# Kernel tuning notes

Hardware: AMD Instinct MI355X
Metric: run time of the kernel (lower is better)

The kernel has to match this reference:

```python
import jax, jax.numpy as jnp
import numpy as np

SEQ, DM, STATE, BATCH = 1024, 512, 16, 8
D2 = 2 * DM
EPS = 1e-5


def rmsnorm(x, w):
    return x * jax.lax.rsqrt(jnp.mean(x * x, axis=-1, keepdims=True) + EPS) * w


def setup_inputs() -> dict:
    key = jax.random.key(0)
    ks = jax.random.split(key, 16)
    def lin(k, i, o):
        k1, k2 = jax.random.split(k)
        s = 1.0 / np.sqrt(i)
        return (jax.random.uniform(k1, (i, o), minval=-s, maxval=s),
                jax.random.uniform(k2, (o,), minval=-s, maxval=s))
    inp_w, inp_b = lin(ks[0], DM, D2)
    convlin_w, convlin_b = lin(ks[1], D2, D2)
    fc1_w, fc1_b = lin(ks[2], D2, D2)
    fc2_w, fc2_b = lin(ks[3], D2, STATE)
    fc3_w, fc3_b = lin(ks[4], D2, STATE)
    D_w, D_b = lin(ks[5], DM, D2)
    out_w, _ = lin(ks[6], D2, DM)
    out_b = jnp.ones((DM,))  # nn.init.constant_(out_proj.bias, 1.0)
    # Conv1d(seq_len, seq_len, k=3): weight (out_ch=SEQ, in_ch=SEQ, 3)
    s = 1.0 / np.sqrt(SEQ * 3)
    conv_w = jax.random.uniform(ks[7], (SEQ, SEQ, 3), minval=-s, maxval=s)
    conv_b = jax.random.uniform(ks[8], (SEQ,), minval=-s, maxval=s)
    norm_w = jnp.ones((DM,))
    x = jax.random.normal(ks[9], (BATCH, SEQ, DM))
    return dict(x=x, norm_w=norm_w, inp_w=inp_w, inp_b=inp_b, conv_w=conv_w,
                conv_b=conv_b, convlin_w=convlin_w, convlin_b=convlin_b,
                fc1_w=fc1_w, fc1_b=fc1_b, fc2_w=fc2_w, fc2_b=fc2_b,
                fc3_w=fc3_w, fc3_b=fc3_b, D_w=D_w, D_b=D_b,
                out_w=out_w, out_b=out_b)


def reference(x, norm_w, inp_w, inp_b, conv_w, conv_b, convlin_w, convlin_b,
              fc1_w, fc1_b, fc2_w, fc2_b, fc3_w, fc3_b, D_w, D_b, out_w, out_b):
    xn = rmsnorm(x, norm_w)                                  # (b, L, d)
    x_proj = xn @ inp_w + inp_b                              # (b, L, 2d)
    # Conv1d over channels=seq_len, spatial=2d, padding=1
    x_conv = jax.lax.conv_general_dilated(
        x_proj, conv_w, window_strides=(1,), padding=[(1, 1)],
        dimension_numbers=('NCH', 'OIH', 'NCH')) + conv_b[None, :, None]
    x_conv_out = jax.nn.silu(x_conv) @ convlin_w + convlin_b  # (b, L, 2d)
    # S6: h starts at zero so dA term vanishes; y = x*delta*sum_n(B*C)
    u = x_conv_out
    B = u @ fc2_w + fc2_b                                     # (b, L, n)
    C = u @ fc3_w + fc3_b                                     # (b, L, n)
    delta = jax.nn.softplus(u @ fc1_w + fc1_b)                # (b, L, 2d)
    bc = jnp.sum(B * C, axis=-1, keepdims=True)               # (b, L, 1)
    x_ssm = u * delta * bc                                    # (b, L, 2d)
    x_act = jax.nn.silu(x_ssm)
    x_residual = jax.nn.silu(xn @ D_w + D_b)
    return (x_residual * x_act) @ out_w + out_b               # (b, L, d)
```

## Files before the change

kernel.cpp:

```cpp
#include <hip/hip_runtime.h>
#include <hip/hip_bf16.h>

#define SEQ 1024
#define DM 512
#define D2 1024
#define NSTATE 16
#define BATCH 8
#define ROWS (BATCH * SEQ)
#define EPSF 1e-5f

typedef __attribute__((ext_vector_type(8))) short bf16x8;
typedef __attribute__((ext_vector_type(4))) float f32x4;

#define AS1 __attribute__((address_space(1)))
#define AS3 __attribute__((address_space(3)))

__device__ __forceinline__ void gll16(const void* g, void* l) {
    __builtin_amdgcn_global_load_lds(
        (const AS1 unsigned int*)(uintptr_t)g,
        (AS3 unsigned int*)(unsigned int)(uintptr_t)l, 16, 0, 0);
}

__device__ __forceinline__ float sigmoidf_(float x) {
    return 1.f / (1.f + __expf(-x));
}
__device__ __forceinline__ unsigned short f2bf(float f) {
    __hip_bfloat16 h = __float2bfloat16(f);
    unsigned short r;
    __builtin_memcpy(&r, &h, 2);
    return r;
}

__global__ __launch_bounds__(256) void prep_all(
    const float* s0, const float* s1, const float* s2, const float* s3,
    const float* s4, const float* s5, const float* s6,
    __hip_bfloat16* d0, __hip_bfloat16* d1, __hip_bfloat16* d2,
    __hip_bfloat16* d3, __hip_bfloat16* d4, __hip_bfloat16* d5,
    __hip_bfloat16* d6) {
    const int j = blockIdx.z;
    int R, C;
    const float* src;
    __hip_bfloat16* dst;
    switch (j) {
        case 0: src = s0; dst = d0; R = 512; C = 1024; break;
        case 1: src = s1; dst = d1; R = 512; C = 1024; break;
        case 2: src = s2; dst = d2; R = 1024; C = 1024; break;
        case 3: src = s3; dst = d3; R = 1024; C = 1024; break;
        case 4: src = s4; dst = d4; R = 1024; C = 512; break;
        case 5: src = s5; dst = d5; R = 1024; C = 16; break;
        default: src = s6; dst = d6; R = 1024; C = 16; break;
    }
    int c0 = blockIdx.x * 32, r0 = blockIdx.y * 32;
    if (c0 >= C || r0 >= R) return;
    __shared__ float tile[32][33];
    int tx = threadIdx.x & 31, ty = threadIdx.x >> 5;
#pragma unroll
    for (int p = 0; p < 4; ++p) {
        int r = r0 + ty + p * 8, c = c0 + tx;
        if (r < R && c < C) tile[ty + p * 8][tx] = src[(size_t)r * C + c];
    }
    __syncthreads();
#pragma unroll
    for (int p = 0; p < 4; ++p) {
        int c = c0 + ty + p * 8, r = r0 + tx;
        if (r < R && c < C)
            dst[(size_t)c * R + r] = __float2bfloat16(tile[tx][ty + p * 8]);
    }
}

__global__ __launch_bounds__(256) void convw_k(const float* __restrict__ cw,
                                               __hip_bfloat16* __restrict__ wk) {
    int idx = blockIdx.x * 256 + threadIdx.x;
    float a = cw[(size_t)idx * 3 + 0];
    float b = cw[(size_t)idx * 3 + 1];
    float c = cw[(size_t)idx * 3 + 2];
    wk[idx] = __float2bfloat16(a);
    wk[(size_t)SEQ * SEQ + idx] = __float2bfloat16(b);
    wk[(size_t)2 * SEQ * SEQ + idx] = __float2bfloat16(c);
}

__global__ __launch_bounds__(256) void rmsnorm_k(
    const float* __restrict__ x, const float* __restrict__ w,
    __hip_bfloat16* __restrict__ o) {
    int row = blockIdx.x;
    const float* xr = x + (size_t)row * DM;
    __hip_bfloat16* orow = o + (size_t)row * DM;
    int t = threadIdx.x;
    float v0 = xr[t];
    float v1 = xr[t + 256];
    float ss = v0 * v0 + v1 * v1;
#pragma unroll
    for (int off = 32; off; off >>= 1) ss += __shfl_down(ss, off, 64);
    __shared__ float parts[4];
    if ((t & 63) == 0) parts[t >> 6] = ss;
    __syncthreads();
    float tot = parts[0] + parts[1] + parts[2] + parts[3];
    float rs = rsqrtf(tot * (1.f / DM) + EPSF);
    orow[t] = __float2bfloat16(v0 * rs * w[t]);
    orow[t + 256] = __float2bfloat16(v1 * rs * w[t + 256]);
}

template <int EPI, int KC>
__global__ __launch_bounds__(256) void mgemm(
    const __hip_bfloat16* __restrict__ A, const __hip_bfloat16* __restrict__ Bt,
    const float* __restrict__ bias, void* __restrict__ outp,
    void* __restrict__ outp2, const float* __restrict__ bias2,
    const __hip_bfloat16* __restrict__ uptr,
    const __hip_bfloat16* __restrict__ resid, const float* __restrict__ bcv,
    int M, int N) {
    __shared__ __align__(16) __hip_bfloat16 As[4][128 * 32];
    __shared__ __align__(16) __hip_bfloat16 Bs[4][128 * 32];
    const int nbx = gridDim.x;
    int lin = blockIdx.y * nbx + blockIdx.x;
    int chunk = (nbx * gridDim.y) >> 3;
    int wg = (lin & 7) * chunk + (lin >> 3);
    const int n0 = (wg % nbx) * 128, m0 = (wg / nbx) * 128;
    const int t = threadIdx.x, lane = t & 63, w = t >> 6;
    const int wr = w >> 1, wc = w & 1;
    const int l15 = lane & 15, l4 = lane >> 4;

    const int r0_ = t >> 2, c0_ = (t & 3) ^ ((r0_ >> 1) & 3);
    const int b1 = 256 + t, r1_ = b1 >> 2, c1_ = (b1 & 3) ^ ((r1_ >> 1) & 3);
    const __hip_bfloat16* gA0 = A + (size_t)(m0 + r0_) * KC + c0_ * 8;
    const __hip_bfloat16* gA1 = A + (size_t)(m0 + r1_) * KC + c1_ * 8;
    const __hip_bfloat16* gB0 = Bt + (size_t)(n0 + r0_) * KC + c0_ * 8;
    const __hip_bfloat16* gB1 = Bt + (size_t)(n0 + r1_) * KC + c1_ * 8;
    const int d0 = (w * 64) * 8, d1 = (256 + w * 64) * 8;

    int offA[4], offB[4];
#pragma unroll
    for (int i = 0; i < 4; ++i) {
        int ra = wr * 64 + i * 16 + l15;
        offA[i] = (ra * 4 + (l4 ^ ((ra >> 1) & 3))) * 8;
        int rb = wc * 64 + i * 16 + l15;
        offB[i] = (rb * 4 + (l4 ^ ((rb >> 1) & 3))) * 8;
    }

#define MSTAGE(BUF, K0)                  \
    {                                    \
        gll16(gA0 + (K0), &As[BUF][d0]); \
        gll16(gA1 + (K0), &As[BUF][d1]); \
        gll16(gB0 + (K0), &Bs[BUF][d0]); \
        gll16(gB1 + (K0), &Bs[BUF][d1]); \
    }

    f32x4 acc[4][4] = {};
    constexpr int NT = KC >> 6;
    MSTAGE(0, 0);
    MSTAGE(1, 32);
    asm volatile("s_waitcnt vmcnt(0)" ::: "memory");
    __builtin_amdgcn_s_barrier();
    __builtin_amdgcn_sched_barrier(0);

#pragma unroll 1
    for (int p = 0; p < NT; ++p) {
        const int kA = 2 * p, kB = 2 * p + 1;
        const int bufA = kA & 3, bufB = kB & 3;
        if (p + 1 < NT) {
            MSTAGE((kA + 2) & 3, (kA + 2) * 32);
            MSTAGE((kB + 2) & 3, (kB + 2) * 32);
        }
        bf16x8 a0[4], b0[4], a1[4], b1v[4];
#pragma unroll
        for (int i = 0; i < 4; ++i) {
            a0[i] = *(const bf16x8*)&As[bufA][offA[i]];
            b0[i] = *(const bf16x8*)&Bs[bufA][offB[i]];
        }
#pragma unroll
        for (int i = 0; i < 4; ++i) {
            a1[i] = *(const bf16x8*)&As[bufB][offA[i]];
            b1v[i] = *(const bf16x8*)&Bs[bufB][offB[i]];
        }
        __builtin_amdgcn_s_setprio(1);
#pragma unroll
        for (int i = 0; i < 4; ++i)
#pragma unroll
            for (int j = 0; j < 4; ++j)
                acc[i][j] = __builtin_amdgcn_mfma_f32_16x16x32_bf16(
                    a0[i], b0[j], acc[i][j], 0, 0, 0);
#pragma unroll
        for (int i = 0; i < 4; ++i)
#pragma unroll
            for (int j = 0; j < 4; ++j)
                acc[i][j] = __builtin_amdgcn_mfma_f32_16x16x32_bf16(
                    a1[i], b1v[j], acc[i][j], 0, 0, 0);
        __builtin_amdgcn_s_setprio(0);
        if (p + 1 < NT) {
            asm volatile("s_waitcnt vmcnt(0)" ::: "memory");
            __builtin_amdgcn_s_barrier();
            __builtin_amdgcn_sched_barrier(0);
        }
    }
#undef MSTAGE

    const int mb = m0 + wr * 64, nb = n0 + wc * 64;
#pragma unroll
    for (int i = 0; i < 4; ++i) {
#pragma unroll
        for (int j = 0; j < 4; ++j) {
            int ngl = nb + j * 16 + l15;
            if (EPI == 5) {
                if (nb < D2) {
                    float bj = bias[ngl];
                    int b = m0 >> 10;
                    int ibase = (mb & (SEQ - 1)) + i * 16 + l4 * 4;
                    ushort4 pk;
                    pk.x = f2bf(acc[i][j][0] + bj);
                    pk.y = f2bf(acc[i][j][1] + bj);
                    pk.z = f2bf(acc[i][j][2] + bj);
                    pk.w = f2bf(acc[i][j][3] + bj);
                    *(ushort4*)((__hip_bfloat16*)outp +
                                ((size_t)b * D2 + ngl) * SEQ + ibase) = pk;
                } else {
                    int ng2 = ngl - D2;
                    float bj = bias2[ng2];
#pragma unroll
                    for (int r = 0; r < 4; ++r) {
                        int mg = mb + i * 16 + l4 * 4 + r;
                        float c = acc[i][j][r] + bj;
                        ((__hip_bfloat16*)outp2)[(size_t)mg * D2 + ng2] =
                            __float2bfloat16(c * sigmoidf_(c));
                    }
                }
            } else {
                float bj = bias[ngl];
#pragma unroll
                for (int r = 0; r < 4; ++r) {
                    int mg = mb + i * 16 + l4 * 4 + r;
                    size_t ro = (size_t)mg * N + ngl;
                    float c = acc[i][j][r] + bj;
                    if (EPI == 1) {
                        ((__hip_bfloat16*)outp)[ro] = __float2bfloat16(c);
                    } else if (EPI == 3) {
                        float sp = (c > 20.f) ? c : log1pf(__expf(c));
                        float xs = __bfloat162float(uptr[ro]) * sp * bcv[mg];
                        float v = __bfloat162float(resid[ro]) *
                                  (xs * sigmoidf_(xs));
                        ((__hip_bfloat16*)outp)[ro] = __float2bfloat16(v);
                    } else {
                        ((float*)outp)[ro] = c;
                    }
                }
            }
        }
    }
}

__global__ __launch_bounds__(256) void conv_mfma(
    const __hip_bfloat16* __restrict__ wk,
    const __hip_bfloat16* __restrict__ Xt,
    const float* __restrict__ cb, __hip_bfloat16* __restrict__ outp) {
    __shared__ __align__(16) __hip_bfloat16 Ws[2][3][128 * 32];
    __shared__ __align__(16) __hip_bfloat16 Xs[2][128 * 32];
    __shared__ __align__(16) __hip_bfloat16 Xh[2][SEQ];
    int lin = blockIdx.x + 8 * blockIdx.y + 64 * blockIdx.z;
    int wg = (lin & 7) * 64 + (lin >> 3);
    const int n0 = (wg & 7) * 128;
    const int m0 = ((wg >> 3) & 7) * 128;
    const int z = wg >> 6;
    const int t = threadIdx.x, lane = t & 63, w = t >> 6;
    const int wr = w >> 1, wc = w & 1;
    const int l15 = lane & 15, l4 = lane >> 4;
    const __hip_bfloat16* Xtb = Xt + (size_t)z * D2 * SEQ;

    {
        int which = t >> 7;
        int col = (t & 127) * 8;
        int h = n0 - 1 + which * 129;
        uint4 v = make_uint4(0u, 0u, 0u, 0u);
        if (h >= 0 && h < D2)
            v = *(const uint4*)(Xtb + (size_t)h * SEQ + col);
        *(uint4*)&Xh[which][col] = v;
    }

    int rowp[2], cbw[2];
#pragma unroll
    for (int p = 0; p < 2; ++p) {
        int blk = p * 256 + t;
        rowp[p] = blk >> 2;
        cbw[p] = (blk & 3) ^ ((rowp[p] >> 1) & 3);
    }
    const __hip_bfloat16* wsrc[2][3];
    const __hip_bfloat16* xsrc[2];
#pragma unroll
    for (int p = 0; p < 2; ++p) {
#pragma unroll
        for (int tp = 0; tp < 3; ++tp)
            wsrc[p][tp] = wk + (size_t)tp * SEQ * SEQ +
                          (size_t)(m0 + rowp[p]) * SEQ + cbw[p] * 8;
        xsrc[p] = Xtb + (size_t)(n0 + rowp[p]) * SEQ + cbw[p] * 8;
    }
    const int dst0 = (w * 64) * 8, dst1 = (256 + w * 64) * 8;

    int offA[4];
#pragma unroll
    for (int i = 0; i < 4; ++i) {
        int ra = wr * 64 + i * 16 + l15;
        offA[i] = (ra * 4 + (l4 ^ ((ra >> 1) & 3))) * 8;
    }

#define CSTAGE(BUF, K0)                              \
    {                                                \
        gll16(wsrc[0][0] + (K0), &Ws[BUF][0][dst0]); \
        gll16(wsrc[1][0] + (K0), &Ws[BUF][0][dst1]); \
        gll16(wsrc[0][1] + (K0), &Ws[BUF][1][dst0]); \
        gll16(wsrc[1][1] + (K0), &Ws[BUF][1][dst1]); \
        gll16(wsrc[0][2] + (K0), &Ws[BUF][2][dst0]); \
        gll16(wsrc[1][2] + (K0), &Ws[BUF][2][dst1]); \
        gll16(xsrc[0] + (K0), &Xs[BUF][dst0]);       \
        gll16(xsrc[1] + (K0), &Xs[BUF][dst1]);       \
    }

    f32x4 acc[4][4] = {};
    CSTAGE(0, 0);
    asm volatile("s_waitcnt lgkmcnt(0)" ::: "memory");

#pragma unroll 1
    for (int kt = 0; kt < 32; ++kt) {
        const int k0 = kt * 32;
        const int buf = kt & 1;
        if (kt + 1 < 32) {
            CSTAGE(buf ^ 1, (kt + 1) * 32);
            asm volatile("s_waitcnt vmcnt(8)" ::: "memory");
        } else {
            asm volatile("s_waitcnt vmcnt(0)" ::: "memory");
        }
        __builtin_amdgcn_s_barrier();
        __builtin_amdgcn_sched_barrier(0);
        bf16x8 aw[3][4];
#pragma unroll
        for (int tp = 0; tp < 3; ++tp)
#pragma unroll
            for (int i = 0; i < 4; ++i)
                aw[tp][i] = *(const bf16x8*)&Ws[buf][tp][offA[i]];
        __builtin_amdgcn_s_setprio(1);
#pragma unroll
        for (int j = 0; j < 4; ++j) {
#pragma unroll
            for (int tp = 0; tp < 3; ++tp) {
                int rb = wc * 64 + j * 16 + l15 + tp;
                int r = rb - 1;
                const __hip_bfloat16* src =
                    &Xs[buf][(r * 4 + (l4 ^ ((r >> 1) & 3))) * 8];
                if (rb == 0) src = &Xh[0][k0 + l4 * 8];
                if (rb == 129) src = &Xh[1][k0 + l4 * 8];
                bf16x8 bvx = *(const bf16x8*)src;
#pragma unroll
                for (int i = 0; i < 4; ++i)
                    acc[i][j] = __builtin_amdgcn_mfma_f32_16x16x32_bf16(
                        aw[tp][i], bvx, acc[i][j], 0, 0, 0);
            }
        }
        __builtin_amdgcn_s_setprio(0);
        if (kt + 1 < 32) {
            __builtin_amdgcn_s_barrier();
            __builtin_amdgcn_sched_barrier(0);
        }
    }
#undef CSTAGE

    const int mb = m0 + wr * 64, nb = n0 + wc * 64;
    size_t ob = (size_t)z * SEQ * D2;
#pragma unroll
    for (int i = 0; i < 4; ++i)
#pragma unroll
        for (int j = 0; j < 4; ++j)
#pragma unroll
            for (int r = 0; r < 4; ++r) {
                int mg = mb + i * 16 + l4 * 4 + r;
                int ng = nb + j * 16 + l15;
                float c = acc[i][j][r] + cb[mg];
                outp[ob + (size_t)mg * D2 + ng] =
                    __float2bfloat16(c * sigmoidf_(c));
            }
}

__global__ __launch_bounds__(256) void bc2_k(
    const __hip_bfloat16* __restrict__ u, const __hip_bfloat16* __restrict__ fcT,
    const float* __restrict__ b2, const float* __restrict__ b3,
    float* __restrict__ bc) {
    __shared__ __align__(16) __hip_bfloat16 Bl[32 * 1024];
    __shared__ __align__(16) __hip_bfloat16 As[3][128 * 32];
    const int m0 = blockIdx.x * 128;
    const int t = threadIdx.x, lane = t & 63, w = t >> 6;
    const int l15 = lane & 15, l4 = lane >> 4;

#pragma unroll
    for (int it = 0; it < 16; ++it) {
        int q = it * 256 + t;
        int n = q >> 7, blk = q & 127;
        uint4 v = *(const uint4*)(fcT + (size_t)n * 1024 + blk * 8);
        *(uint4*)&Bl[(n * 128 + (blk ^ (n & 7))) * 8] = v;
    }

    const int r0_ = t >> 2, c0_ = (t & 3) ^ ((r0_ >> 1) & 3);
    const int bq = 256 + t, r1_ = bq >> 2, c1_ = (bq & 3) ^ ((r1_ >> 1) & 3);
    const __hip_bfloat16* gA0 = u + (size_t)(m0 + r0_) * 1024 + c0_ * 8;
    const __hip_bfloat16* gA1 = u + (size_t)(m0 + r1_) * 1024 + c1_ * 8;
    const int d0 = (w * 64) * 8, d1 = (256 + w * 64) * 8;

    int offA[2];
#pragma unroll
    for (int i = 0; i < 2; ++i) {
        int ra = w * 32 + i * 16 + l15;
        offA[i] = (ra * 4 + (l4 ^ ((ra >> 1) & 3))) * 8;
    }

#define BSTAGE(BUF, K0)                  \
    {                                    \
        gll16(gA0 + (K0), &As[BUF][d0]); \
        gll16(gA1 + (K0), &As[BUF][d1]); \
    }

    f32x4 acc[2][2] = {};
    unsigned curb = 0, nxtb = 1, thdb = 2;
    BSTAGE(0, 0);
    BSTAGE(1, 32);
    asm volatile("s_waitcnt vmcnt(2)" ::: "memory");
    __builtin_amdgcn_s_barrier();
    __builtin_amdgcn_sched_barrier(0);

#pragma unroll 1
    for (int kt = 0; kt < 32; ++kt) {
        const bool st = (kt + 2 < 32);
        if (st) BSTAGE(thdb, (kt + 2) * 32);
        bf16x8 af[2], bf[2];
#pragma unroll
        for (int i = 0; i < 2; ++i) af[i] = *(const bf16x8*)&As[curb][offA[i]];
#pragma unroll
        for (int nj = 0; nj < 2; ++nj) {
            int n = nj * 16 + l15;
            int blk = (kt * 4 + l4) ^ (n & 7);
            bf[nj] = *(const bf16x8*)&Bl[(n * 128 + blk) * 8];
        }
#pragma unroll
        for (int i = 0; i < 2; ++i)
#pragma unroll
            for (int nj = 0; nj < 2; ++nj)
                acc[i][nj] = __builtin_amdgcn_mfma_f32_16x16x32_bf16(
                    af[i], bf[nj], acc[i][nj], 0, 0, 0);
        if (kt + 1 < 32) {
            if (st)
                asm volatile("s_waitcnt vmcnt(2)" ::: "memory");
            else
                asm volatile("s_waitcnt vmcnt(0)" ::: "memory");
            __builtin_amdgcn_s_barrier();
            __builtin_amdgcn_sched_barrier(0);
        }
        unsigned tb = curb;
        curb = nxtb;
        nxtb = thdb;
        thdb = tb;
    }
#undef BSTAGE

    float bb2 = b2[l15], bb3 = b3[l15];
#pragma unroll
    for (int i = 0; i < 2; ++i)
#pragma unroll
        for (int r = 0; r < 4; ++r) {
            float Bv = acc[i][0][r] + bb2;
            float Cv = acc[i][1][r] + bb3;
            float p = Bv * Cv;
            p += __shfl_xor(p, 1, 64);
            p += __shfl_xor(p, 2, 64);
            p += __shfl_xor(p, 4, 64);
            p += __shfl_xor(p, 8, 64);
            if (l15 == 0)
                bc[m0 + w * 32 + i * 16 + l4 * 4 + r] = p;
        }
}

extern "C" void kernel_launch(void* const* d_in, const int* in_sizes, int n_in,
                              void* d_out, int out_size, void* d_ws,
                              size_t ws_size, hipStream_t stream) {
    const float* x = (const float*)d_in[0];
    const float* norm_w = (const float*)d_in[1];
    const float* inp_w = (const float*)d_in[2];
    const float* inp_b = (const float*)d_in[3];
    const float* conv_w = (const float*)d_in[4];
    const float* conv_b = (const float*)d_in[5];
    const float* convlin_w = (const float*)d_in[6];
    const float* convlin_b = (const float*)d_in[7];
    const float* fc1_w = (const float*)d_in[8];
    const float* fc1_b = (const float*)d_in[9];
    const float* fc2_w = (const float*)d_in[10];
    const float* fc2_b = (const float*)d_in[11];
    const float* fc3_w = (const float*)d_in[12];
    const float* fc3_b = (const float*)d_in[13];
    const float* D_w = (const float*)d_in[14];
    const float* D_b = (const float*)d_in[15];
    const float* out_w = (const float*)d_in[16];
    const float* out_b = (const float*)d_in[17];
    float* out = (float*)d_out;

    __hip_bfloat16* xnb = (__hip_bfloat16*)d_ws;
    __hip_bfloat16* xt = xnb + (size_t)ROWS * DM;
    __hip_bfloat16* cvo = xt + (size_t)BATCH * D2 * SEQ;
    __hip_bfloat16* u = cvo + (size_t)ROWS * D2;
    __hip_bfloat16* resid = u + (size_t)ROWS * D2;
    __hip_bfloat16* Wcat = resid + (size_t)ROWS * D2;
    __hip_bfloat16* clT = Wcat + (size_t)2 * D2 * DM;
    __hip_bfloat16* fc1T = clT + (size_t)D2 * D2;
    __hip_bfloat16* outT = fc1T + (size_t)D2 * D2;
    __hip_bfloat16* wk = outT + (size_t)DM * D2;
    __hip_bfloat16* fcT = wk + (size_t)3 * SEQ * SEQ;
    float* bcb = (float*)(fcT + (size_t)32 * D2);

    prep_all<<<dim3(32, 32, 7), 256, 0, stream>>>(
        inp_w, D_w, convlin_w, fc1_w, out_w, fc2_w, fc3_w, Wcat,
        Wcat + (size_t)D2 * DM, clT, fc1T, outT, fcT, fcT + (size_t)16 * D2);
    convw_k<<<SEQ * SEQ / 256, 256, 0, stream>>>(conv_w, wk);
    rmsnorm_k<<<ROWS, 256, 0, stream>>>(x, norm_w, xnb);
    mgemm<5, DM><<<dim3(2 * D2 / 128, ROWS / 128), 256, 0, stream>>>(
        xnb, Wcat, inp_b, xt, resid, D_b, nullptr, nullptr, nullptr, ROWS,
        2 * D2);
    conv_mfma<<<dim3(D2 / 128, SEQ / 128, BATCH), 256, 0, stream>>>(
        wk, xt, conv_b, cvo);
    mgemm<1, D2><<<dim3(D2 / 128, ROWS / 128), 256, 0, stream>>>(
        cvo, clT, convlin_b, u, nullptr, nullptr, nullptr, nullptr, nullptr,
        ROWS, D2);
    bc2_k<<<ROWS / 128, 256, 0, stream>>>(u, fcT, fc2_b, fc3_b, bcb);
    mgemm<3, D2><<<dim3(D2 / 128, ROWS / 128), 256, 0, stream>>>(
        u, fc1T, fc1_b, cvo, nullptr, nullptr, u, resid, bcb, ROWS, D2);
    mgemm<4, D2><<<dim3(DM / 128, ROWS / 128), 256, 0, stream>>>(
        cvo, outT, out_b, out, nullptr, nullptr, nullptr, nullptr, nullptr,
        ROWS, DM);
}
```

Baseline: 224.4 us.

## Fold convlin weights into fc1/fc2/fc3 and fuse u and delta GEMMs

```diff
diff --git a/kernel.cpp b/kernel.cpp
--- a/kernel.cpp
+++ b/kernel.cpp
@@ -24,20 +24,54 @@
 __device__ __forceinline__ float sigmoidf_(float x) {
     return 1.f / (1.f + __expf(-x));
 }
+__device__ __forceinline__ float softplusf_(float x) {
+    return fmaxf(x, 0.f) + __logf(1.f + __expf(-fabsf(x)));
+}
 __device__ __forceinline__ unsigned short f2bf(float f) {
     __hip_bfloat16 h = __float2bfloat16(f);
     unsigned short r;
     __builtin_memcpy(&r, &h, 2);
     return r;
 }
+__device__ __forceinline__ float bf2f(__hip_bfloat16 h) {
+    return __bfloat162float(h);
+}
+__device__ __forceinline__ float bfbits2f(short s) {
+    return __uint_as_float(((unsigned)(unsigned short)s) << 16);
+}
 
 __global__ __launch_bounds__(256) void prep_all(
     const float* s0, const float* s1, const float* s2, const float* s3,
-    const float* s4, const float* s5, const float* s6,
-    __hip_bfloat16* d0, __hip_bfloat16* d1, __hip_bfloat16* d2,
-    __hip_bfloat16* d3, __hip_bfloat16* d4, __hip_bfloat16* d5,
-    __hip_bfloat16* d6) {
+    const float* s4, const float* s5, const float* s6, const float* clw,
+    const float* cw, __hip_bfloat16* d0, __hip_bfloat16* d1,
+    __hip_bfloat16* d2, __hip_bfloat16* d3, __hip_bfloat16* d4,
+    __hip_bfloat16* d5, __hip_bfloat16* d6, __hip_bfloat16* clB,
+    __hip_bfloat16* wk) {
     const int j = blockIdx.z;
+    if (j == 8) {
+        int bid = blockIdx.y * 32 + blockIdx.x;
+        int base = bid * 1024 + threadIdx.x;
+#pragma unroll
+        for (int it = 0; it < 4; ++it) {
+            int idx = base + it * 256;
+            wk[idx] = __float2bfloat16(cw[(size_t)idx * 3 + 0]);
+            wk[(size_t)SEQ * SEQ + idx] =
+                __float2bfloat16(cw[(size_t)idx * 3 + 1]);
+            wk[(size_t)2 * SEQ * SEQ + idx] =
+                __float2bfloat16(cw[(size_t)idx * 3 + 2]);
+        }
+        return;
+    }
+    if (j == 7) {
+        int c0 = blockIdx.x * 32, r0 = blockIdx.y * 32;
+        int tx = threadIdx.x & 31, ty = threadIdx.x >> 5;
+#pragma unroll
+        for (int p = 0; p < 4; ++p) {
+            int r = r0 + ty + p * 8, c = c0 + tx;
+            clB[(size_t)r * D2 + c] = __float2bfloat16(clw[(size_t)r * D2 + c]);
+        }
+        return;
+    }
     int R, C;
     const float* src;
     __hip_bfloat16* dst;
@@ -68,15 +102,46 @@
     }
 }
 
-__global__ __launch_bounds__(256) void convw_k(const float* __restrict__ cw,
-                                               __hip_bfloat16* __restrict__ wk) {
-    int idx = blockIdx.x * 256 + threadIdx.x;
-    float a = cw[(size_t)idx * 3 + 0];
-    float b = cw[(size_t)idx * 3 + 1];
-    float c = cw[(size_t)idx * 3 + 2];
-    wk[idx] = __float2bfloat16(a);
-    wk[(size_t)SEQ * SEQ + idx] = __float2bfloat16(b);
-    wk[(size_t)2 * SEQ * SEQ + idx] = __float2bfloat16(c);
+__global__ __launch_bounds__(256) void biasprep_k(
+    const float* __restrict__ clb, const float* __restrict__ fc1w,
+    const float* __restrict__ fc1b, const float* __restrict__ fc2w,
+    const float* __restrict__ fc2b, const float* __restrict__ fc3w,
+    const float* __restrict__ fc3b, float* __restrict__ b1p,
+    float* __restrict__ b23p) {
+    int g = blockIdx.x * 256 + threadIdx.x;
+    if (g < 1024) {
+        float acc = 0.f;
+        for (int k = 0; k < 1024; ++k) acc += clb[k] * fc1w[(size_t)k * 1024 + g];
+        b1p[g] = acc + fc1b[g];
+    } else if (g < 1040) {
+        int s = g - 1024;
+        float acc = 0.f;
+        for (int k = 0; k < 1024; ++k) acc += clb[k] * fc2w[k * 16 + s];
+        b23p[s] = acc + fc2b[s];
+    } else if (g < 1056) {
+        int s = g - 1040;
+        float acc = 0.f;
+        for (int k = 0; k < 1024; ++k) acc += clb[k] * fc3w[k * 16 + s];
+        b23p[16 + s] = acc + fc3b[s];
+    }
+}
+
+__global__ __launch_bounds__(256) void prepw23_k(
+    const __hip_bfloat16* __restrict__ clB, const __hip_bfloat16* __restrict__ fcT,
+    __hip_bfloat16* __restrict__ W2pT) {
+    int g = blockIdx.x * 256 + threadIdx.x;
+    int k = g >> 5, s = g & 31;
+    const __hip_bfloat16* ck = clB + (size_t)k * 1024;
+    const __hip_bfloat16* fs = fcT + (size_t)s * 1024;
+    float acc = 0.f;
+    for (int j = 0; j < 1024; j += 8) {
+        bf16x8 a = *(const bf16x8*)&ck[j];
+        bf16x8 b = *(const bf16x8*)&fs[j];
+#pragma unroll
+        for (int e = 0; e < 8; ++e)
+            acc += bfbits2f(a[e]) * bfbits2f(b[e]);
+    }
+    W2pT[(size_t)s * 1024 + k] = __float2bfloat16(acc);
 }
 
 __global__ __launch_bounds__(256) void rmsnorm_k(
@@ -104,10 +169,7 @@
 __global__ __launch_bounds__(256) void mgemm(
     const __hip_bfloat16* __restrict__ A, const __hip_bfloat16* __restrict__ Bt,
     const float* __restrict__ bias, void* __restrict__ outp,
-    void* __restrict__ outp2, const float* __restrict__ bias2,
-    const __hip_bfloat16* __restrict__ uptr,
-    const __hip_bfloat16* __restrict__ resid, const float* __restrict__ bcv,
-    int M, int N) {
+    void* __restrict__ outp2, const float* __restrict__ bias2, int M, int N) {
     __shared__ __align__(16) __hip_bfloat16 As[4][128 * 32];
     __shared__ __align__(16) __hip_bfloat16 Bs[4][128 * 32];
     const int nbx = gridDim.x;
@@ -223,20 +285,14 @@
                     }
                 }
             } else {
-                float bj = bias[ngl];
+                float bj = (EPI == 6) ? 0.f : bias[ngl];
 #pragma unroll
                 for (int r = 0; r < 4; ++r) {
                     int mg = mb + i * 16 + l4 * 4 + r;
                     size_t ro = (size_t)mg * N + ngl;
                     float c = acc[i][j][r] + bj;
-                    if (EPI == 1) {
+                    if (EPI == 6) {
                         ((__hip_bfloat16*)outp)[ro] = __float2bfloat16(c);
-                    } else if (EPI == 3) {
-                        float sp = (c > 20.f) ? c : log1pf(__expf(c));
-                        float xs = __bfloat162float(uptr[ro]) * sp * bcv[mg];
-                        float v = __bfloat162float(resid[ro]) *
-                                  (xs * sigmoidf_(xs));
-                        ((__hip_bfloat16*)outp)[ro] = __float2bfloat16(v);
                     } else {
                         ((float*)outp)[ro] = c;
                     }
@@ -244,6 +300,214 @@
             }
         }
     }
+}
+
+__global__ __launch_bounds__(256) void fused_ud(
+    const __hip_bfloat16* __restrict__ A, const __hip_bfloat16* __restrict__ BtU,
+    const __hip_bfloat16* __restrict__ BtD, const float* __restrict__ biasU,
+    const float* __restrict__ biasD, const __hip_bfloat16* __restrict__ resid,
+    const float* __restrict__ bcv, __hip_bfloat16* __restrict__ act) {
+    __shared__ __align__(16) __hip_bfloat16 As[2][128 * 32];
+    __shared__ __align__(16) __hip_bfloat16 Bu[2][128 * 32];
+    __shared__ __align__(16) __hip_bfloat16 Bd[2][128 * 32];
+    const int nbx = gridDim.x;
+    int lin = blockIdx.y * nbx + blockIdx.x;
+    int chunk = (nbx * gridDim.y) >> 3;
+    int wg = (lin & 7) * chunk + (lin >> 3);
+    const int n0 = (wg % nbx) * 128, m0 = (wg / nbx) * 128;
+    const int t = threadIdx.x, lane = t & 63, w = t >> 6;
+    const int wr = w >> 1, wc = w & 1;
+    const int l15 = lane & 15, l4 = lane >> 4;
+
+    const int r0_ = t >> 2, c0_ = (t & 3) ^ ((r0_ >> 1) & 3);
+    const int b1 = 256 + t, r1_ = b1 >> 2, c1_ = (b1 & 3) ^ ((r1_ >> 1) & 3);
+    const __hip_bfloat16* gA0 = A + (size_t)(m0 + r0_) * D2 + c0_ * 8;
+    const __hip_bfloat16* gA1 = A + (size_t)(m0 + r1_) * D2 + c1_ * 8;
+    const __hip_bfloat16* gU0 = BtU + (size_t)(n0 + r0_) * D2 + c0_ * 8;
+    const __hip_bfloat16* gU1 = BtU + (size_t)(n0 + r1_) * D2 + c1_ * 8;
+    const __hip_bfloat16* gD0 = BtD + (size_t)(n0 + r0_) * D2 + c0_ * 8;
+    const __hip_bfloat16* gD1 = BtD + (size_t)(n0 + r1_) * D2 + c1_ * 8;
+    const int d0 = (w * 64) * 8, d1 = (256 + w * 64) * 8;
+
+    int offA[4], offB[4];
+#pragma unroll
+    for (int i = 0; i < 4; ++i) {
+        int ra = wr * 64 + i * 16 + l15;
+        offA[i] = (ra * 4 + (l4 ^ ((ra >> 1) & 3))) * 8;
+        int rb = wc * 64 + i * 16 + l15;
+        offB[i] = (rb * 4 + (l4 ^ ((rb >> 1) & 3))) * 8;
+    }
+
+#define FSTAGE(BUF, K0)                  \
+    {                                    \
+        gll16(gA0 + (K0), &As[BUF][d0]); \
+        gll16(gA1 + (K0), &As[BUF][d1]); \
+        gll16(gU0 + (K0), &Bu[BUF][d0]); \
+        gll16(gU1 + (K0), &Bu[BUF][d1]); \
+        gll16(gD0 + (K0), &Bd[BUF][d0]); \
+        gll16(gD1 + (K0), &Bd[BUF][d1]); \
+    }
+
+    f32x4 accU[4][4] = {};
+    f32x4 accD[4][4] = {};
+    FSTAGE(0, 0);
+
+#pragma unroll 1
+    for (int kt = 0; kt < 32; ++kt) {
+        const int buf = kt & 1;
+        if (kt + 1 < 32) {
+            FSTAGE(buf ^ 1, (kt + 1) * 32);
+            asm volatile("s_waitcnt vmcnt(6)" ::: "memory");
+        } else {
+            asm volatile("s_waitcnt vmcnt(0)" ::: "memory");
+        }
+        __builtin_amdgcn_s_barrier();
+        __builtin_amdgcn_sched_barrier(0);
+        bf16x8 af[4], bu[4], bd[4];
+#pragma unroll
+        for (int i = 0; i < 4; ++i) {
+            af[i] = *(const bf16x8*)&As[buf][offA[i]];
+            bu[i] = *(const bf16x8*)&Bu[buf][offB[i]];
+            bd[i] = *(const bf16x8*)&Bd[buf][offB[i]];
+        }
+        __builtin_amdgcn_s_setprio(1);
+#pragma unroll
+        for (int i = 0; i < 4; ++i)
+#pragma unroll
+            for (int j = 0; j < 4; ++j)
+                accU[i][j] = __builtin_amdgcn_mfma_f32_16x16x32_bf16(
+                    af[i], bu[j], accU[i][j], 0, 0, 0);
+#pragma unroll
+        for (int i = 0; i < 4; ++i)
+#pragma unroll
+            for (int j = 0; j < 4; ++j)
+                accD[i][j] = __builtin_amdgcn_mfma_f32_16x16x32_bf16(
+                    af[i], bd[j], accD[i][j], 0, 0, 0);
+        __builtin_amdgcn_s_setprio(0);
+        if (kt + 1 < 32) {
+            __builtin_amdgcn_s_barrier();
+            __builtin_amdgcn_sched_barrier(0);
+        }
+    }
+#undef FSTAGE
+
+    const int mb = m0 + wr * 64, nb = n0 + wc * 64;
+#pragma unroll
+    for (int i = 0; i < 4; ++i) {
+#pragma unroll
+        for (int j = 0; j < 4; ++j) {
+            int ngl = nb + j * 16 + l15;
+            float bU = biasU[ngl];
+            float bD = biasD[ngl];
+#pragma unroll
+            for (int r = 0; r < 4; ++r) {
+                int mg = mb + i * 16 + l4 * 4 + r;
+                size_t ro = (size_t)mg * D2 + ngl;
+                float cu = accU[i][j][r] + bU;
+                float cd = accD[i][j][r] + bD;
+                float sp = softplusf_(cd);
+                float xs = cu * sp * bcv[mg];
+                float v = bf2f(resid[ro]) * (xs * sigmoidf_(xs));
+                act[ro] = __float2bfloat16(v);
+            }
+        }
+    }
+}
+
+__global__ __launch_bounds__(256) void bc2_k(
+    const __hip_bfloat16* __restrict__ u, const __hip_bfloat16* __restrict__ fcT,
+    const float* __restrict__ b2, const float* __restrict__ b3,
+    float* __restrict__ bc) {
+    __shared__ __align__(16) __hip_bfloat16 Bl[32 * 1024];
+    __shared__ __align__(16) __hip_bfloat16 As[3][128 * 32];
+    const int m0 = blockIdx.x * 128;
+    const int t = threadIdx.x, lane = t & 63, w = t >> 6;
+    const int l15 = lane & 15, l4 = lane >> 4;
+
+#pragma unroll
+    for (int it = 0; it < 16; ++it) {
+        int q = it * 256 + t;
+        int n = q >> 7, blk = q & 127;
+        uint4 v = *(const uint4*)(fcT + (size_t)n * 1024 + blk * 8);
+        *(uint4*)&Bl[(n * 128 + (blk ^ (n & 7))) * 8] = v;
+    }
+
+    const int r0_ = t >> 2, c0_ = (t & 3) ^ ((r0_ >> 1) & 3);
+    const int bq = 256 + t, r1_ = bq >> 2, c1_ = (bq & 3) ^ ((r1_ >> 1) & 3);
+    const __hip_bfloat16* gA0 = u + (size_t)(m0 + r0_) * 1024 + c0_ * 8;
+    const __hip_bfloat16* gA1 = u + (size_t)(m0 + r1_) * 1024 + c1_ * 8;
+    const int d0 = (w * 64) * 8, d1 = (256 + w * 64) * 8;
+
+    int offA[2];
+#pragma unroll
+    for (int i = 0; i < 2; ++i) {
+        int ra = w * 32 + i * 16 + l15;
+        offA[i] = (ra * 4 + (l4 ^ ((ra >> 1) & 3))) * 8;
+    }
+
+#define BSTAGE(BUF, K0)                  \
+    {                                    \
+        gll16(gA0 + (K0), &As[BUF][d0]); \
+        gll16(gA1 + (K0), &As[BUF][d1]); \
+    }
+
+    f32x4 acc[2][2] = {};
+    unsigned curb = 0, nxtb = 1, thdb = 2;
+    BSTAGE(0, 0);
+    BSTAGE(1, 32);
+    asm volatile("s_waitcnt vmcnt(2)" ::: "memory");
+    __builtin_amdgcn_s_barrier();
+    __builtin_amdgcn_sched_barrier(0);
+
+#pragma unroll 1
+    for (int kt = 0; kt < 32; ++kt) {
+        const bool st = (kt + 2 < 32);
+        if (st) BSTAGE(thdb, (kt + 2) * 32);
+        bf16x8 af[2], bf[2];
+#pragma unroll
+        for (int i = 0; i < 2; ++i) af[i] = *(const bf16x8*)&As[curb][offA[i]];
+#pragma unroll
+        for (int nj = 0; nj < 2; ++nj) {
+            int n = nj * 16 + l15;
+            int blk = (kt * 4 + l4) ^ (n & 7);
+            bf[nj] = *(const bf16x8*)&Bl[(n * 128 + blk) * 8];
+        }
+#pragma unroll
+        for (int i = 0; i < 2; ++i)
+#pragma unroll
+            for (int nj = 0; nj < 2; ++nj)
+                acc[i][nj] = __builtin_amdgcn_mfma_f32_16x16x32_bf16(
+                    af[i], bf[nj], acc[i][nj], 0, 0, 0);
+        if (kt + 1 < 32) {
+            if (st)
+                asm volatile("s_waitcnt vmcnt(2)" ::: "memory");
+            else
+                asm volatile("s_waitcnt vmcnt(0)" ::: "memory");
+            __builtin_amdgcn_s_barrier();
+            __builtin_amdgcn_sched_barrier(0);
+        }
+        unsigned tb = curb;
+        curb = nxtb;
+        nxtb = thdb;
+        thdb = tb;
+    }
+#undef BSTAGE
+
+    float bb2 = b2[l15], bb3 = b3[l15];
+#pragma unroll
+    for (int i = 0; i < 2; ++i)
+#pragma unroll
+        for (int r = 0; r < 4; ++r) {
+            float Bv = acc[i][0][r] + bb2;
+            float Cv = acc[i][1][r] + bb3;
+            float p = Bv * Cv;
+            p += __shfl_xor(p, 1, 64);
+            p += __shfl_xor(p, 2, 64);
+            p += __shfl_xor(p, 4, 64);
+            p += __shfl_xor(p, 8, 64);
+            if (l15 == 0)
+                bc[m0 + w * 32 + i * 16 + l4 * 4 + r] = p;
+        }
 }
 
 __global__ __launch_bounds__(256) void conv_mfma(
@@ -373,102 +637,6 @@
                 outp[ob + (size_t)mg * D2 + ng] =
                     __float2bfloat16(c * sigmoidf_(c));
             }
-}
-
-__global__ __launch_bounds__(256) void bc2_k(
-    const __hip_bfloat16* __restrict__ u, const __hip_bfloat16* __restrict__ fcT,
-    const float* __restrict__ b2, const float* __restrict__ b3,
-    float* __restrict__ bc) {
-    __shared__ __align__(16) __hip_bfloat16 Bl[32 * 1024];
-    __shared__ __align__(16) __hip_bfloat16 As[3][128 * 32];
-    const int m0 = blockIdx.x * 128;
-    const int t = threadIdx.x, lane = t & 63, w = t >> 6;
-    const int l15 = lane & 15, l4 = lane >> 4;
-
-#pragma unroll
-    for (int it = 0; it < 16; ++it) {
-        int q = it * 256 + t;
-        int n = q >> 7, blk = q & 127;
-        uint4 v = *(const uint4*)(fcT + (size_t)n * 1024 + blk * 8);
-        *(uint4*)&Bl[(n * 128 + (blk ^ (n & 7))) * 8] = v;
-    }
-
-    const int r0_ = t >> 2, c0_ = (t & 3) ^ ((r0_ >> 1) & 3);
-    const int bq = 256 + t, r1_ = bq >> 2, c1_ = (bq & 3) ^ ((r1_ >> 1) & 3);
-    const __hip_bfloat16* gA0 = u + (size_t)(m0 + r0_) * 1024 + c0_ * 8;
-    const __hip_bfloat16* gA1 = u + (size_t)(m0 + r1_) * 1024 + c1_ * 8;
-    const int d0 = (w * 64) * 8, d1 = (256 + w * 64) * 8;
-
-    int offA[2];
-#pragma unroll
-    for (int i = 0; i < 2; ++i) {
-        int ra = w * 32 + i * 16 + l15;
-        offA[i] = (ra * 4 + (l4 ^ ((ra >> 1) & 3))) * 8;
-    }
-
-#define BSTAGE(BUF, K0)                  \
-    {                                    \
-        gll16(gA0 + (K0), &As[BUF][d0]); \
-        gll16(gA1 + (K0), &As[BUF][d1]); \
-    }
-
-    f32x4 acc[2][2] = {};
-    unsigned curb = 0, nxtb = 1, thdb = 2;
-    BSTAGE(0, 0);
-    BSTAGE(1, 32);
-    asm volatile("s_waitcnt vmcnt(2)" ::: "memory");
-    __builtin_amdgcn_s_barrier();
-    __builtin_amdgcn_sched_barrier(0);
-
-#pragma unroll 1
-    for (int kt = 0; kt < 32; ++kt) {
-        const bool st = (kt + 2 < 32);
-        if (st) BSTAGE(thdb, (kt + 2) * 32);
-        bf16x8 af[2], bf[2];
-#pragma unroll
-        for (int i = 0; i < 2; ++i) af[i] = *(const bf16x8*)&As[curb][offA[i]];
-#pragma unroll
-        for (int nj = 0; nj < 2; ++nj) {
-            int n = nj * 16 + l15;
-            int blk = (kt * 4 + l4) ^ (n & 7);
-            bf[nj] = *(const bf16x8*)&Bl[(n * 128 + blk) * 8];
-        }
-#pragma unroll
-        for (int i = 0; i < 2; ++i)
-#pragma unroll
-            for (int nj = 0; nj < 2; ++nj)
-                acc[i][nj] = __builtin_amdgcn_mfma_f32_16x16x32_bf16(
-                    af[i], bf[nj], acc[i][nj], 0, 0, 0);
-        if (kt + 1 < 32) {
-            if (st)
-                asm volatile("s_waitcnt vmcnt(2)" ::: "memory");
-            else
-                asm volatile("s_waitcnt vmcnt(0)" ::: "memory");
-            __builtin_amdgcn_s_barrier();
-            __builtin_amdgcn_sched_barrier(0);
-        }
-        unsigned tb = curb;
-        curb = nxtb;
-        nxtb = thdb;
-        thdb = tb;
-    }
-#undef BSTAGE
-
-    float bb2 = b2[l15], bb3 = b3[l15];
-#pragma unroll
-    for (int i = 0; i < 2; ++i)
-#pragma unroll
-        for (int r = 0; r < 4; ++r) {
-            float Bv = acc[i][0][r] + bb2;
-            float Cv = acc[i][1][r] + bb3;
-            float p = Bv * Cv;
-            p += __shfl_xor(p, 1, 64);
-            p += __shfl_xor(p, 2, 64);
-            p += __shfl_xor(p, 4, 64);
-            p += __shfl_xor(p, 8, 64);
-            if (l15 == 0)
-                bc[m0 + w * 32 + i * 16 + l4 * 4 + r] = p;
-        }
 }
 
 extern "C" void kernel_launch(void* const* d_in, const int* in_sizes, int n_in,
@@ -497,33 +665,38 @@
     __hip_bfloat16* xnb = (__hip_bfloat16*)d_ws;
     __hip_bfloat16* xt = xnb + (size_t)ROWS * DM;
     __hip_bfloat16* cvo = xt + (size_t)BATCH * D2 * SEQ;
-    __hip_bfloat16* u = cvo + (size_t)ROWS * D2;
-    __hip_bfloat16* resid = u + (size_t)ROWS * D2;
+    __hip_bfloat16* act = cvo + (size_t)ROWS * D2;
+    __hip_bfloat16* resid = act + (size_t)ROWS * D2;
     __hip_bfloat16* Wcat = resid + (size_t)ROWS * D2;
     __hip_bfloat16* clT = Wcat + (size_t)2 * D2 * DM;
     __hip_bfloat16* fc1T = clT + (size_t)D2 * D2;
     __hip_bfloat16* outT = fc1T + (size_t)D2 * D2;
     __hip_bfloat16* wk = outT + (size_t)DM * D2;
     __hip_bfloat16* fcT = wk + (size_t)3 * SEQ * SEQ;
-    float* bcb = (float*)(fcT + (size_t)32 * D2);
-
-    prep_all<<<dim3(32, 32, 7), 256, 0, stream>>>(
-        inp_w, D_w, convlin_w, fc1_w, out_w, fc2_w, fc3_w, Wcat,
-        Wcat + (size_t)D2 * DM, clT, fc1T, outT, fcT, fcT + (size_t)16 * D2);
-    convw_k<<<SEQ * SEQ / 256, 256, 0, stream>>>(conv_w, wk);
+    __hip_bfloat16* clB = fcT + (size_t)32 * D2;
+    __hip_bfloat16* W1pT = clB + (size_t)D2 * D2;
+    __hip_bfloat16* W2pT = W1pT + (size_t)D2 * D2;
+    float* b1p = (float*)(W2pT + (size_t)32 * D2);
+    float* b23p = b1p + D2;
+    float* bcb = b23p + 32;
+
+    prep_all<<<dim3(32, 32, 9), 256, 0, stream>>>(
+        inp_w, D_w, convlin_w, fc1_w, out_w, fc2_w, fc3_w, convlin_w, conv_w,
+        Wcat, Wcat + (size_t)D2 * DM, clT, fc1T, outT, fcT,
+        fcT + (size_t)16 * D2, clB, wk);
+    biasprep_k<<<5, 256, 0, stream>>>(convlin_b, fc1_w, fc1_b, fc2_w, fc2_b,
+                                      fc3_w, fc3_b, b1p, b23p);
+    mgemm<6, D2><<<dim3(D2 / 128, D2 / 128), 256, 0, stream>>>(
+        fc1T, clB, nullptr, W1pT, nullptr, nullptr, D2, D2);
+    prepw23_k<<<128, 256, 0, stream>>>(clB, fcT, W2pT);
     rmsnorm_k<<<ROWS, 256, 0, stream>>>(x, norm_w, xnb);
     mgemm<5, DM><<<dim3(2 * D2 / 128, ROWS / 128), 256, 0, stream>>>(
-        xnb, Wcat, inp_b, xt, resid, D_b, nullptr, nullptr, nullptr, ROWS,
-        2 * D2);
+        xnb, Wcat, inp_b, xt, resid, D_b, ROWS, 2 * D2);
     conv_mfma<<<dim3(D2 / 128, SEQ / 128, BATCH), 256, 0, stream>>>(
         wk, xt, conv_b, cvo);
-    mgemm<1, D2><<<dim3(D2 / 128, ROWS / 128), 256, 0, stream>>>(
-        cvo, clT, convlin_b, u, nullptr, nullptr, nullptr, nullptr, nullptr,
-        ROWS, D2);
-    bc2_k<<<ROWS / 128, 256, 0, stream>>>(u, fcT, fc2_b, fc3_b, bcb);
-    mgemm<3, D2><<<dim3(D2 / 128, ROWS / 128), 256, 0, stream>>>(
-        u, fc1T, fc1_b, cvo, nullptr, nullptr, u, resid, bcb, ROWS, D2);
+    bc2_k<<<ROWS / 128, 256, 0, stream>>>(cvo, W2pT, b23p, b23p + 16, bcb);
+    fused_ud<<<dim3(D2 / 128, ROWS / 128), 256, 0, stream>>>(
+        cvo, clT, W1pT, convlin_b, b1p, resid, bcb, act);
     mgemm<4, D2><<<dim3(DM / 128, ROWS / 128), 256, 0, stream>>>(
-        cvo, outT, out_b, out, nullptr, nullptr, nullptr, nullptr, nullptr,
-        ROWS, DM);
-}
+        act, outT, out_b, out, nullptr, nullptr, ROWS, DM);
+}
```

Result: slower. 304.5 us (+35.7%).
